# Performance work log

Hardware: AMD Instinct MI355X
Metric: run time of the kernel (lower is better)

The kernel has to match this reference:

```python
import jax, jax.numpy as jnp
import numpy as np
import math

B, L, T, NW, D, DL = 4, 48, 16, 20, 256, 64


def setup_inputs() -> dict:
    key = jax.random.key(0)
    ks = jax.random.split(key, 16)
    n = lambda k, s, sc=1.0: jax.random.normal(k, s, dtype=jnp.float32) * sc
    z = lambda s: jnp.zeros(s, dtype=jnp.float32)
    return {
        'f_c': n(ks[0], (B, L, L, T, D), 0.5),
        'f_m': n(ks[1], (B, L, L, D), 0.5),
        'f_b': n(ks[2], (B, L, D), 0.5),
        'f_w': n(ks[3], (B, NW, D), 0.5),
        'f_s': n(ks[4], (B, D), 0.5),
        'bWq': n(ks[5], (D, D), 0.02), 'bbq': z((D,)),
        'bWk': n(ks[6], (D, D), 0.02), 'bbk': z((D,)),
        'cWq': n(ks[7], (DL, DL), 0.05), 'cbq': z((DL,)),
        'cWk': n(ks[8], (DL, DL), 0.05), 'cbk': z((DL,)),
        'dcc_w': n(ks[9], (DL, D), 0.05), 'dcc_b': z((DL,)),
        'dcw_w': n(ks[10], (DL, D), 0.05), 'dcw_b': z((DL,)),
        'dcs_w': n(ks[11], (DL, D), 0.05), 'dcs_b': z((DL,)),
        'ucc_w': n(ks[12], (D, DL), 0.05), 'ucc_b': z((D,)),
        'mfb_w': n(ks[13], (L, L), 0.05), 'mfb_b': z((L,)),
        'mfc_w': n(ks[14], (L, L), 0.05), 'mfc_b': z((L,)),
    }


def _smi_forward(f_c, f_m, f_b, f_w, f_s, bWq, bbq, bWk, bbk, cWq, cbq, cWk, cbk,
                 dcc_w, dcc_b, dcw_w, dcw_b, dcs_w, dcs_b, ucc_w, ucc_b,
                 mfb_w, mfb_b, mfc_w, mfc_b):
    lin = lambda x, W, b: x @ W.T + b  # torch Linear / 1x1 conv over channel-last

    def boundary_unit(fb, fm):
        # cross attention over words
        q = lin(fb, bWq, bbq)                                   # (B,L,D)
        k = lin(f_w, bWk, bbk)                                  # (B,Nw,D)
        aw = jax.nn.softmax(jnp.einsum('bld,bnd->bln', q, k) / math.sqrt(D), axis=-1)
        f_baq = jnp.einsum('bln,bnd->bld', aw, f_w)
        f_bq = fb * (f_baq + f_s[:, None, :])
        A_b = jax.nn.softmax(jnp.einsum('bld,bmd->blm', f_bq, f_bq) / math.sqrt(D), axis=-1)
        f_bb = jnp.einsum('blm,bmd->bld', A_b, fb)
        g_m = jax.nn.sigmoid(fm * f_s[:, None, None, :])        # (B,L,L,D)
        f_bm = jnp.einsum('blm,blmd->bld', A_b, g_m * fm)
        return f_bb + fb + f_bm

    def content_unit(fc, fm):
        f_c_hat = lin(fc, dcc_w, dcc_b)                         # (B,L,L,T,dl)
        f_w_hat = lin(f_w, dcw_w, dcw_b)                        # (B,Nw,dl)
        f_s_hat = lin(f_s, dcs_w, dcs_b)                        # (B,dl)
        q = lin(f_c_hat, cWq, cbq)
        k = lin(f_w_hat, cWk, cbk)
        aw = jax.nn.softmax(jnp.einsum('blmtd,bnd->blmtn', q, k) / math.sqrt(DL), axis=-1)
        f_caq = jnp.einsum('blmtn,bnd->blmtd', aw, f_w_hat)
        f_cq = f_c_hat * (f_caq + f_s_hat[:, None, None, None, :])
        A_c = jax.nn.softmax(jnp.einsum('blmtd,blmsd->blmts', f_cq, f_cq) / math.sqrt(DL), axis=-1)
        f_cc_hat = jnp.einsum('blmts,blmsd->blmtd', A_c, f_c_hat)
        f_cc = lin(f_cc_hat, ucc_w, ucc_b)                      # (B,L,L,T,D)
        g_m = jax.nn.sigmoid(fm * f_s[:, None, None, :])
        return f_cc + fc + (g_m * fm)[:, :, :, None, :]

    def moment_unit(fc, fm, fb):
        prod = fb[:, :, None, :] * fb[:, None, :, :]            # (B,L,L,D)
        conv_fb = jnp.einsum('oi,bimd->bomd', mfb_w, prod) + mfb_b[None, :, None, None]
        fc_mean = jnp.mean(fc, axis=3)                          # (B,L,L,D)
        conv_fc = jnp.einsum('oi,bimd->bomd', mfc_w, fc_mean) + mfc_b[None, :, None, None]
        return conv_fb + conv_fc + fm

    cu, bu, mu = f_c, f_b, f_m
    for _ in range(3):
        cu_n = content_unit(cu, mu)
        bu_n = boundary_unit(bu, mu)
        mu = moment_unit(cu_n, mu, bu_n)
        cu, bu = cu_n, bu_n
    return (mu, bu)


def reference(f_c, f_m, f_b, f_w, f_s, bWq, bbq, bWk, bbk, cWq, cbq, cWk, cbk,
              dcc_w, dcc_b, dcw_w, dcw_b, dcs_w, dcs_b, ucc_w, ucc_b,
              mfb_w, mfb_b, mfc_w, mfc_b):
    return _smi_forward(f_c, f_m, f_b, f_w, f_s, bWq, bbq, bWk, bbk, cWq, cbq, cWk, cbk,
                        dcc_w, dcc_b, dcw_w, dcw_b, dcs_w, dcs_b, ucc_w, ucc_b,
                        mfb_w, mfb_b, mfc_w, mfc_b)
```

## Files before the change

### kernel.cpp

```cpp
#include <hip/hip_runtime.h>

#define BB 4
#define LL 48
#define TT 16
#define NWW 20
#define DD 256
#define DLL 64

typedef __attribute__((ext_vector_type(8))) short s8v;
typedef __attribute__((ext_vector_type(4))) float f4v;
typedef unsigned short ushort_t;

#define FENCE() asm volatile("" ::: "memory")

#define OFF_CU     0ull
#define OFF_CM     75497472ull
#define OFF_BU0    84934656ull
#define OFF_BU1    85131264ull
#define OFF_FBQ    85327872ull
#define OFF_FWH    85524480ull
#define OFF_FSH    85544960ull
#define OFF_KB     85545984ull
#define OFF_BWQT   85627904ull
#define OFF_WBT    85890048ull
#define OFF_WCT    85899264ull
#define OFF_DCCF   85908480ull
#define OFF_CWQF   85941248ull
#define OFF_UCCF   85949440ull
#define OFF_KCF    85982208ull
#define OFF_FWHTF  85998592ull

static __device__ __forceinline__ ushort_t f2bf(float f){
  unsigned u = __float_as_uint(f);
  return (ushort_t)((u + 0x7FFFu + ((u>>16)&1u)) >> 16);
}
static __device__ __forceinline__ float bf2f(ushort_t h){
  return __uint_as_float(((unsigned)h)<<16);
}
static __device__ __forceinline__ void st64(void* p, float a, float b, float c, float d){
  uint2 v; v.x = (unsigned)f2bf(a) | ((unsigned)f2bf(b)<<16);
  v.y = (unsigned)f2bf(c) | ((unsigned)f2bf(d)<<16);
  *(uint2*)p = v;
}

#define ADR64(row, cb) (((row)<<7) + ((cb) ^ (((row)&7)<<4)))
#define ADR32(row, cb) (((row)<<6) + ((cb) ^ (((row)&3)<<4)))

#define MFMA(a,b,c) __builtin_amdgcn_mfma_f32_16x16x32_bf16((a),(b),(c),0,0,0)

template<int FIRST>
__global__ __launch_bounds__(256)
void content_kernel(const void* cusrc_, ushort_t* cudst, float* __restrict__ cm,
                    const float* __restrict__ fm_src, const float* __restrict__ fsg,
                    const float* __restrict__ fsh, const float* __restrict__ dccb,
                    const float* __restrict__ cbq, const float* __restrict__ uccb,
                    const ushort_t* __restrict__ dccf, const ushort_t* __restrict__ cwqf,
                    const ushort_t* __restrict__ uccf, const ushort_t* __restrict__ kcf,
                    const ushort_t* __restrict__ fwhtf)
{
  __shared__ __align__(16) char sm_all[4][8192];
  const int wid = threadIdx.x >> 6;
  const int lane = threadIdx.x & 63;
  char* sm = sm_all[wid];
  const int t = lane & 15, g = lane >> 4;
  const int tile = blockIdx.x*4 + wid;
  const int b = tile / (LL*LL);

  {
    f4v z = {0.f,0.f,0.f,0.f};
    *(f4v*)(sm + 4096 + ADR32(lane, 32)) = z;
    *(f4v*)(sm + 4096 + ADR32(lane, 48)) = z;
  }

  s8v xb[8];
  if (FIRST){
    const float* xp = (const float*)cusrc_ + (size_t)tile*4096 + t*DD + g*8;
    #pragma unroll
    for (int kk=0;kk<8;kk++){
      f4v lo = *(const f4v*)(xp + kk*32);
      f4v hi = *(const f4v*)(xp + kk*32 + 4);
      s8v v;
      v[0]=(short)f2bf(lo[0]); v[1]=(short)f2bf(lo[1]);
      v[2]=(short)f2bf(lo[2]); v[3]=(short)f2bf(lo[3]);
      v[4]=(short)f2bf(hi[0]); v[5]=(short)f2bf(hi[1]);
      v[6]=(short)f2bf(hi[2]); v[7]=(short)f2bf(hi[3]);
      xb[kk]=v;
    }
  } else {
    const ushort_t* xp = (const ushort_t*)cusrc_ + (size_t)tile*4096 + lane*8;
    #pragma unroll
    for (int kk=0;kk<8;kk++) xb[kk] = *(const s8v*)(xp + kk*512);
  }

  f4v accH[4];
  {
    f4v z = {0.f,0.f,0.f,0.f};
    accH[0]=z; accH[1]=z; accH[2]=z; accH[3]=z;
  }
  #pragma unroll
  for (int kk=0;kk<8;kk++){
    #pragma unroll
    for (int m0=0;m0<4;m0++){
      s8v a = *(const s8v*)(dccf + (((m0<<3)+kk)<<9) + (lane<<3));
      accH[m0] = MFMA(a, xb[kk], accH[m0]);
    }
  }
  s8v cwa[8];
  #pragma unroll
  for (int i=0;i<8;i++) cwa[i] = *(const s8v*)(cwqf + (i<<9) + (lane<<3));
  #pragma unroll
  for (int m0=0;m0<4;m0++){
    f4v acc = accH[m0];
    f4v bi = *(const f4v*)(dccb + m0*16 + g*4);
    acc[0]+=bi[0]; acc[1]+=bi[1]; acc[2]+=bi[2]; acc[3]+=bi[3];
    accH[m0]=acc;
    st64(sm + ADR64(t, m0*32 + g*8), acc[0],acc[1],acc[2],acc[3]);
    #pragma unroll
    for (int r=0;r<4;r++)
      *(ushort_t*)(sm + 4096 + ADR32(m0*16 + g*4 + r, t*2)) = f2bf(acc[r]);
  }
  FENCE();

  s8v hb0 = *(const s8v*)(sm + ADR64(t, g*16));
  s8v hb1 = *(const s8v*)(sm + ADR64(t, 64 + g*16));
  #pragma unroll
  for (int m0=0;m0<4;m0++){
    f4v acc = {0.f,0.f,0.f,0.f};
    acc = MFMA(cwa[m0*2  ], hb0, acc);
    acc = MFMA(cwa[m0*2+1], hb1, acc);
    f4v bi = *(const f4v*)(cbq + m0*16 + g*4);
    st64(sm + 2048 + ADR64(t, m0*32 + g*8),
         acc[0]+bi[0], acc[1]+bi[1], acc[2]+bi[2], acc[3]+bi[3]);
  }
  s8v kca[4];
  #pragma unroll
  for (int i=0;i<4;i++) kca[i] = *(const s8v*)(kcf + (b<<11) + (i<<9) + (lane<<3));
  FENCE();

  s8v qb0 = *(const s8v*)(sm + 2048 + ADR64(t, g*16));
  s8v qb1 = *(const s8v*)(sm + 2048 + ADR64(t, 64 + g*16));
  f4v sA[2];
  #pragma unroll
  for (int m0=0;m0<2;m0++){
    f4v acc = {0.f,0.f,0.f,0.f};
    acc = MFMA(kca[m0*2  ], qb0, acc);
    acc = MFMA(kca[m0*2+1], qb1, acc);
    sA[m0]=acc;
  }
  float mx = -3.0e38f;
  #pragma unroll
  for (int m0=0;m0<2;m0++){
    #pragma unroll
    for (int r=0;r<4;r++){
      int n = m0*16 + g*4 + r;
      if (n < NWW) mx = fmaxf(mx, sA[m0][r]);
    }
  }
  mx = fmaxf(mx, __shfl_xor(mx, 16));
  mx = fmaxf(mx, __shfl_xor(mx, 32));
  float ex[8]; float sum = 0.f;
  #pragma unroll
  for (int m0=0;m0<2;m0++){
    #pragma unroll
    for (int r=0;r<4;r++){
      int n = m0*16 + g*4 + r;
      float e = (n < NWW) ? __expf(sA[m0][r]-mx) : 0.f;
      ex[m0*4+r]=e; sum+=e;
    }
  }
  sum += __shfl_xor(sum,16);
  sum += __shfl_xor(sum,32);
  float inv = 1.f/sum;
  #pragma unroll
  for (int m0=0;m0<2;m0++)
    st64(sm + ADR32(t, m0*32 + g*8),
         ex[m0*4]*inv, ex[m0*4+1]*inv, ex[m0*4+2]*inv, ex[m0*4+3]*inv);
  s8v fwa[4];
  #pragma unroll
  for (int i=0;i<4;i++) fwa[i] = *(const s8v*)(fwhtf + (b<<11) + (i<<9) + (lane<<3));
  FENCE();

  s8v awb = *(const s8v*)(sm + ADR32(t, g*16));
  FENCE();
  #pragma unroll
  for (int m0=0;m0<4;m0++){
    f4v z = {0.f,0.f,0.f,0.f};
    f4v acc = MFMA(fwa[m0], awb, z);
    f4v fv = *(const f4v*)(fsh + b*DLL + m0*16 + g*4);
    float cq0 = accH[m0][0]*(acc[0]+fv[0])*0.35355339059f;
    float cq1 = accH[m0][1]*(acc[1]+fv[1])*0.35355339059f;
    float cq2 = accH[m0][2]*(acc[2]+fv[2])*0.35355339059f;
    float cq3 = accH[m0][3]*(acc[3]+fv[3])*0.35355339059f;
    ushort_t h0=f2bf(cq0),h1=f2bf(cq1),h2=f2bf(cq2),h3=f2bf(cq3);
    uint2 hv; hv.x=(unsigned)h0|((unsigned)h1<<16); hv.y=(unsigned)h2|((unsigned)h3<<16);
    *(uint2*)(sm + 2048 + ADR64(t, m0*32+g*8)) = hv;
    uint2 lv;
    lv.x = (unsigned)f2bf(cq0-bf2f(h0)) | ((unsigned)f2bf(cq1-bf2f(h1))<<16);
    lv.y = (unsigned)f2bf(cq2-bf2f(h2)) | ((unsigned)f2bf(cq3-bf2f(h3))<<16);
    *(uint2*)(sm + ADR64(t, m0*32+g*8)) = lv;
  }
  FENCE();

  s8v ch0 = *(const s8v*)(sm + 2048 + ADR64(t, g*16));
  s8v ch1 = *(const s8v*)(sm + 2048 + ADR64(t, 64+g*16));
  s8v cl0 = *(const s8v*)(sm + ADR64(t, g*16));
  s8v cl1 = *(const s8v*)(sm + ADR64(t, 64+g*16));
  f4v s2 = {0.f,0.f,0.f,0.f};
  s2 = MFMA(ch0, ch0, s2); s2 = MFMA(ch1, ch1, s2);
  s2 = MFMA(ch0, cl0, s2); s2 = MFMA(ch1, cl1, s2);
  s2 = MFMA(cl0, ch0, s2); s2 = MFMA(cl1, ch1, s2);
  float mx2 = fmaxf(fmaxf(s2[0],s2[1]), fmaxf(s2[2],s2[3]));
  mx2 = fmaxf(mx2, __shfl_xor(mx2,16));
  mx2 = fmaxf(mx2, __shfl_xor(mx2,32));
  float e0=__expf(s2[0]-mx2), e1=__expf(s2[1]-mx2), e2=__expf(s2[2]-mx2), e3=__expf(s2[3]-mx2);
  float su = e0+e1+e2+e3;
  su += __shfl_xor(su,16);
  su += __shfl_xor(su,32);
  float inv2 = 1.f/su;
  FENCE();
  st64(sm + ADR32(t, g*8), e0*inv2, e1*inv2, e2*inv2, e3*inv2);
  { uint2 zz; zz.x=0u; zz.y=0u; *(uint2*)(sm + ADR32(t, 32+g*8)) = zz; }
  FENCE();

  s8v acb = *(const s8v*)(sm + ADR32(t, g*16));
  #pragma unroll
  for (int m0=0;m0<4;m0++){
    s8v a = *(const s8v*)(sm + 4096 + ADR32(m0*16 + t, g*16));
    f4v z = {0.f,0.f,0.f,0.f};
    f4v acc = MFMA(a, acb, z);
    st64(sm + 2048 + ADR64(t, m0*32+g*8), acc[0],acc[1],acc[2],acc[3]);
  }
  FENCE();

  s8v cc0 = *(const s8v*)(sm + 2048 + ADR64(t, g*16));
  s8v cc1 = *(const s8v*)(sm + 2048 + ADR64(t, 64+g*16));
  FENCE();
  const float* fmp = fm_src + (size_t)tile*DD;
  const float* fsp = fsg + b*DD;
  const int frofs = t*8 + (g>>1)*128 + (g&1)*4;
  const ushort_t* xfr = (const ushort_t*)cusrc_ + (size_t)tile*4096 + frofs;
  ushort_t* ofr = cudst + (size_t)tile*4096 + frofs;
  const float* xf = (const float*)cusrc_ + (size_t)tile*4096 + t*DD;
  #pragma unroll
  for (int m0=0;m0<16;m0++){
    f4v acc = {0.f,0.f,0.f,0.f};
    s8v a0 = *(const s8v*)(uccf + (((m0<<1)  )<<9) + (lane<<3));
    s8v a1 = *(const s8v*)(uccf + (((m0<<1)+1)<<9) + (lane<<3));
    acc = MFMA(a0, cc0, acc);
    acc = MFMA(a1, cc1, acc);
    const int dq = m0*16 + g*4;
    const int fi = (m0>>1)*512 + (m0&1)*256;
    f4v ub  = *(const f4v*)(uccb + dq);
    f4v fmv = *(const f4v*)(fmp + dq);
    f4v fvv = *(const f4v*)(fsp + dq);
    float xr0,xr1,xr2,xr3;
    if (FIRST){
      f4v xv = *(const f4v*)(xf + dq);
      xr0=xv[0]; xr1=xv[1]; xr2=xv[2]; xr3=xv[3];
    } else {
      uint2 xv = *(const uint2*)(xfr + fi);
      xr0=bf2f((ushort_t)(xv.x&0xffffu)); xr1=bf2f((ushort_t)(xv.x>>16));
      xr2=bf2f((ushort_t)(xv.y&0xffffu)); xr3=bf2f((ushort_t)(xv.y>>16));
    }
    float o0 = acc[0]+ub[0]+xr0 + fmv[0]*__builtin_amdgcn_rcpf(1.f+__expf(-fmv[0]*fvv[0]));
    float o1 = acc[1]+ub[1]+xr1 + fmv[1]*__builtin_amdgcn_rcpf(1.f+__expf(-fmv[1]*fvv[1]));
    float o2 = acc[2]+ub[2]+xr2 + fmv[2]*__builtin_amdgcn_rcpf(1.f+__expf(-fmv[2]*fvv[2]));
    float o3 = acc[3]+ub[3]+xr3 + fmv[3]*__builtin_amdgcn_rcpf(1.f+__expf(-fmv[3]*fvv[3]));
    uint2 ov; ov.x=(unsigned)f2bf(o0)|((unsigned)f2bf(o1)<<16);
    ov.y=(unsigned)f2bf(o2)|((unsigned)f2bf(o3)<<16);
    *(uint2*)(ofr + fi) = ov;
    *(uint2*)(sm + (t<<9) + ((dq*2) ^ ((t&15)<<3))) = ov;
  }
  FENCE();

  {
    const int d0 = lane*4;
    float s0=0.f,s1=0.f,s2=0.f,s3=0.f;
    #pragma unroll
    for (int tt=0;tt<TT;tt++){
      uint2 v = *(const uint2*)(sm + (tt<<9) + ((d0*2) ^ ((tt&15)<<3)));
      s0 += bf2f((ushort_t)(v.x&0xffffu)); s1 += bf2f((ushort_t)(v.x>>16));
      s2 += bf2f((ushort_t)(v.y&0xffffu)); s3 += bf2f((ushort_t)(v.y>>16));
    }
    f4v o = {s0*0.0625f, s1*0.0625f, s2*0.0625f, s3*0.0625f};
    *(f4v*)(cm + (size_t)tile*DD + d0) = o;
  }
}

__global__ __launch_bounds__(256)
void bnd1_kernel(const float* __restrict__ fb, const float* __restrict__ f_w,
                 const float* __restrict__ f_s, const float* __restrict__ kb,
                 const float* __restrict__ bWqT, const float* __restrict__ bbq,
                 float* __restrict__ fbq)
{
  int blk = blockIdx.x; int b = blk / LL, l = blk % LL;
  int d = threadIdx.x;
  __shared__ float fbrow[DD];
  __shared__ float qrow[DD];
  __shared__ float smx[32];
  fbrow[d] = fb[(size_t)(b*LL+l)*DD + d];
  __syncthreads();
  float q = bbq[d];
  for (int e=0;e<DD;e++) q += fbrow[e]*bWqT[(size_t)e*DD+d];
  qrow[d]=q;
  __syncthreads();
  if (d < NWW){
    float s=0.f; const float* kr = kb + (size_t)(b*NWW+d)*DD;
    for (int e=0;e<DD;e++) s += qrow[e]*kr[e];
    smx[d] = s*(1.0f/16.0f);
  }
  __syncthreads();
  if (d==0){
    float m2=-3.0e38f;
    for(int n=0;n<NWW;n++) m2=fmaxf(m2,smx[n]);
    float su=0.f;
    for(int n=0;n<NWW;n++){ float e=__expf(smx[n]-m2); smx[n]=e; su+=e; }
    float iv=1.f/su;
    for(int n=0;n<NWW;n++) smx[n]*=iv;
  }
  __syncthreads();
  float acc=0.f;
  for (int n=0;n<NWW;n++) acc += smx[n]*f_w[(size_t)(b*NWW+n)*DD+d];
  fbq[(size_t)(b*LL+l)*DD+d] = fbrow[d]*(acc + f_s[b*DD+d]);
}

__global__ __launch_bounds__(256)
void bnd2_kernel(const float* __restrict__ fbq, const float* __restrict__ fb,
                 const float* __restrict__ fm, const float* __restrict__ f_s,
                 float* __restrict__ bu_out)
{
  int blk = blockIdx.x; int b = blk/LL, l = blk%LL;
  int d = threadIdx.x;
  __shared__ float Sl[DD];
  __shared__ float aw[LL];
  Sl[d] = fbq[(size_t)(b*LL+l)*DD + d];
  __syncthreads();
  if (d < LL){
    float s=0.f; const float* fr = fbq + (size_t)(b*LL+d)*DD;
    const f4v* s4 = (const f4v*)Sl; const f4v* f4p = (const f4v*)fr;
    for (int e=0;e<DD/4;e++){
      f4v a=s4[e], c=f4p[e];
      s += a[0]*c[0]+a[1]*c[1]+a[2]*c[2]+a[3]*c[3];
    }
    aw[d] = s*(1.0f/16.0f);
  }
  __syncthreads();
  if (d==0){
    float m2=-3.0e38f;
    for(int n=0;n<LL;n++) m2=fmaxf(m2,aw[n]);
    float su=0.f;
    for(int n=0;n<LL;n++){ float e=__expf(aw[n]-m2); aw[n]=e; su+=e; }
    float iv=1.f/su;
    for(int n=0;n<LL;n++) aw[n]*=iv;
  }
  __syncthreads();
  float fsd = f_s[b*DD+d];
  const float* fmrow = fm + ((size_t)(b*LL+l)*LL)*DD + d;
  float acc=0.f;
  for (int m=0;m<LL;m++){
    float a  = aw[m];
    float fbv= fb[(size_t)(b*LL+m)*DD+d];
    float fmv= fmrow[(size_t)m*DD];
    float gm = 1.f/(1.f+__expf(-fmv*fsd));
    acc += a*(fbv + gm*fmv);
  }
  bu_out[(size_t)(b*LL+l)*DD+d] = acc + fb[(size_t)(b*LL+l)*DD+d];
}

__global__ __launch_bounds__(256)
void moment_kernel(const float* __restrict__ cm, const float* __restrict__ bu,
                   const float* __restrict__ mu_in, float* __restrict__ mu_out,
                   const float* __restrict__ wbT, const float* __restrict__ wcT,
                   const float* __restrict__ mfbb, const float* __restrict__ mfcb)
{
  int blk = blockIdx.x;
  int oh = blk & 1; int bm = blk>>1; int b = bm/LL, m = bm%LL;
  int d = threadIdx.x;
  const int ob = oh*24;
  float accB[24], accC[24];
  #pragma unroll
  for (int o=0;o<24;o++){accB[o]=0.f;accC[o]=0.f;}
  for (int i=0;i<LL;i++){
    float bv = bu[(size_t)(b*LL+i)*DD+d];
    float cv = cm[((size_t)(b*LL+i)*LL+m)*DD+d];
    const float* wb = wbT + i*LL + ob;
    const float* wc = wcT + i*LL + ob;
    #pragma unroll
    for (int o=0;o<24;o+=4){
      f4v w1 = *(const f4v*)(wb+o);
      f4v w2 = *(const f4v*)(wc+o);
      accB[o  ]+=w1[0]*bv; accB[o+1]+=w1[1]*bv; accB[o+2]+=w1[2]*bv; accB[o+3]+=w1[3]*bv;
      accC[o  ]+=w2[0]*cv; accC[o+1]+=w2[1]*cv; accC[o+2]+=w2[2]*cv; accC[o+3]+=w2[3]*cv;
    }
  }
  float bum = bu[(size_t)(b*LL+m)*DD+d];
  #pragma unroll
  for (int o=0;o<24;o++){
    int oo = ob+o;
    size_t oi = ((size_t)(b*LL+oo)*LL+m)*DD + d;
    mu_out[oi] = accB[o]*bum + mfbb[oo] + accC[o] + mfcb[oo] + mu_in[oi];
  }
}

__global__ __launch_bounds__(256)
void prep1_kernel(const float* __restrict__ f_w, const float* __restrict__ f_s,
                  const float* __restrict__ bWq, const float* __restrict__ bWk,
                  const float* __restrict__ bbk,
                  const float* __restrict__ dcw_w, const float* __restrict__ dcw_b,
                  const float* __restrict__ dcs_w, const float* __restrict__ dcs_b,
                  const float* __restrict__ dcc_w, const float* __restrict__ cWq,
                  const float* __restrict__ ucc_w,
                  const float* __restrict__ mfb_w, const float* __restrict__ mfc_w,
                  float* __restrict__ kb, float* __restrict__ fwh,
                  float* __restrict__ fsh, float* __restrict__ bWqT,
                  ushort_t* __restrict__ dccf, ushort_t* __restrict__ cwqf,
                  ushort_t* __restrict__ uccf,
                  float* __restrict__ wbT, float* __restrict__ wcT)
{
  const int S0=20480, S1=5120, S2=256, S3=65536, S4=16384, S5=4096, S6=16384, S7=2304;
  const int TOT = S0+S1+S2+S3+S4+S5+S6+S7;
  int id = blockIdx.x*256 + threadIdx.x;
  int nth = gridDim.x*256;
  for (int x=id; x<TOT; x+=nth){
    int y=x;
    if (y < S0){
      int b=y/(NWW*DD); int r=y%(NWW*DD); int n=r/DD, dd2=r%DD;
      float s=bbk[dd2];
      const float* fr=f_w+(size_t)(b*NWW+n)*DD; const float* wr=bWk+(size_t)dd2*DD;
      for(int e=0;e<DD;e++) s+=fr[e]*wr[e];
      kb[y]=s; continue; }
    y-=S0;
    if (y < S1){
      int b=y/(NWW*DLL); int r=y%(NWW*DLL); int n=r/DLL, dl=r%DLL;
      float s=dcw_b[dl];
      const float* fr=f_w+(size_t)(b*NWW+n)*DD; const float* wr=dcw_w+(size_t)dl*DD;
      for(int e=0;e<DD;e++) s+=fr[e]*wr[e];
      fwh[y]=s; continue; }
    y-=S1;
    if (y < S2){
      int b=y/DLL, dl=y%DLL;
      float s=dcs_b[dl];
      const float* fr=f_s+(size_t)b*DD; const float* wr=dcs_w+(size_t)dl*DD;
      for(int e=0;e<DD;e++) s+=fr[e]*wr[e];
      fsh[y]=s; continue; }
    y-=S2;
    if (y < S3){ int e=y/DD, dd2=y%DD; bWqT[y] = bWq[(size_t)dd2*DD+e]; continue; }
    y-=S3;
    if (y < S4){
      int j=y&7, ln=(y>>3)&63, kk=(y>>9)&7, m0=y>>12;
      int mm=m0*16+(ln&15), k=kk*32+((ln>>4)<<3)+j;
      dccf[y]=f2bf(dcc_w[(size_t)mm*DD+k]); continue; }
    y-=S4;
    if (y < S5){
      int j=y&7, ln=(y>>3)&63, kk=(y>>9)&1, m0=y>>10;
      int mm=m0*16+(ln&15), k=kk*32+((ln>>4)<<3)+j;
      cwqf[y]=f2bf(cWq[(size_t)mm*DLL+k]); continue; }
    y-=S5;
    if (y < S6){
      int j=y&7, ln=(y>>3)&63, kk=(y>>9)&1, m0=y>>10;
      int mm=m0*16+(ln&15), k=kk*32+((ln>>4)<<3)+j;
      uccf[y]=f2bf(ucc_w[(size_t)mm*DLL+k]); continue; }
    y-=S6;
    { int i=y/LL, o=y%LL; wbT[y]=mfb_w[(size_t)o*LL+i]; wcT[y]=mfc_w[(size_t)o*LL+i]; }
  }
}

__global__ __launch_bounds__(256)
void prep2_kernel(const float* __restrict__ fwh, const float* __restrict__ cWk,
                  const float* __restrict__ cbk,
                  ushort_t* __restrict__ kcf, ushort_t* __restrict__ fwhtf)
{
  const int S0 = BB*2048, S1 = BB*2048;
  int id = blockIdx.x*256+threadIdx.x; int nth=gridDim.x*256;
  for (int x=id; x<S0+S1; x+=nth){
    int y=x;
    if (y < S0){
      int b=y>>11; int z=y&2047;
      int j=z&7, ln=(z>>3)&63, kk=(z>>9)&1, m0=z>>10;
      int n=m0*16+(ln&15), k=kk*32+((ln>>4)<<3)+j;
      float v=0.f;
      if (n<NWW){
        float s=cbk[k];
        const float* fr=fwh+(size_t)(b*NWW+n)*DLL; const float* wr=cWk+(size_t)k*DLL;
        for(int e=0;e<DLL;e++) s+=fr[e]*wr[e];
        v=s*0.125f;
      }
      kcf[y]=f2bf(v); continue; }
    y-=S0;
    {
      int b=y>>11; int z=y&2047;
      int j=z&7, ln=(z>>3)&63, m0=z>>9;
      int dl=m0*16+(ln&15), n=((ln>>4)<<3)+j;
      float v = (n<NWW)? fwh[(size_t)(b*NWW+n)*DLL+dl] : 0.f;
      fwhtf[y]=f2bf(v);
    }
  }
}

extern "C" void kernel_launch(void* const* d_in, const int* in_sizes, int n_in,
                              void* d_out, int out_size, void* d_ws, size_t ws_size,
                              hipStream_t stream)
{
  (void)in_sizes; (void)n_in; (void)out_size; (void)ws_size;
  const float* f_c  = (const float*)d_in[0];
  const float* f_m  = (const float*)d_in[1];
  const float* f_b  = (const float*)d_in[2];
  const float* f_w  = (const float*)d_in[3];
  const float* f_s  = (const float*)d_in[4];
  const float* bWq  = (const float*)d_in[5];
  const float* bbq  = (const float*)d_in[6];
  const float* bWk  = (const float*)d_in[7];
  const float* bbk  = (const float*)d_in[8];
  const float* cWq  = (const float*)d_in[9];
  const float* cbq  = (const float*)d_in[10];
  const float* cWk  = (const float*)d_in[11];
  const float* cbk  = (const float*)d_in[12];
  const float* dcc_w= (const float*)d_in[13];
  const float* dcc_b= (const float*)d_in[14];
  const float* dcw_w= (const float*)d_in[15];
  const float* dcw_b= (const float*)d_in[16];
  const float* dcs_w= (const float*)d_in[17];
  const float* dcs_b= (const float*)d_in[18];
  const float* ucc_w= (const float*)d_in[19];
  const float* ucc_b= (const float*)d_in[20];
  const float* mfb_w= (const float*)d_in[21];
  const float* mfb_b= (const float*)d_in[22];
  const float* mfc_w= (const float*)d_in[23];
  const float* mfc_b= (const float*)d_in[24];

  char* ws = (char*)d_ws;
  ushort_t* cu = (ushort_t*)(ws+OFF_CU);
  float* cmr  = (float*)(ws+OFF_CM);
  float* bu0  = (float*)(ws+OFF_BU0);
  float* bu1  = (float*)(ws+OFF_BU1);
  float* fbq  = (float*)(ws+OFF_FBQ);
  float* fwh  = (float*)(ws+OFF_FWH);
  float* fsh  = (float*)(ws+OFF_FSH);
  float* kb   = (float*)(ws+OFF_KB);
  float* bWqT = (float*)(ws+OFF_BWQT);
  float* wbT  = (float*)(ws+OFF_WBT);
  float* wcT  = (float*)(ws+OFF_WCT);
  ushort_t* dccf = (ushort_t*)(ws+OFF_DCCF);
  ushort_t* cwqf = (ushort_t*)(ws+OFF_CWQF);
  ushort_t* uccf = (ushort_t*)(ws+OFF_UCCF);
  ushort_t* kcf  = (ushort_t*)(ws+OFF_KCF);
  ushort_t* fwhtf= (ushort_t*)(ws+OFF_FWHTF);

  float* mu = (float*)d_out;
  float* out_bu = (float*)d_out + 2359296;

  prep1_kernel<<<128,256,0,stream>>>(f_w,f_s,bWq,bWk,bbk,dcw_w,dcw_b,dcs_w,dcs_b,
                                     dcc_w,cWq,ucc_w,mfb_w,mfc_w,
                                     kb,fwh,fsh,bWqT,dccf,cwqf,uccf,wbT,wcT);
  prep2_kernel<<<32,256,0,stream>>>(fwh,cWk,cbk,kcf,fwhtf);

  float* bu_cur = nullptr;
  for (int it=0; it<3; ++it){
    const float* fmsrc = (it==0)? f_m : mu;
    if (it==0)
      content_kernel<1><<<2304,256,0,stream>>>(f_c, cu, cmr, fmsrc, f_s, fsh, dcc_b, cbq, ucc_b,
                                               dccf,cwqf,uccf,kcf,fwhtf);
    else
      content_kernel<0><<<2304,256,0,stream>>>(cu, cu, cmr, fmsrc, f_s, fsh, dcc_b, cbq, ucc_b,
                                               dccf,cwqf,uccf,kcf,fwhtf);
    const float* fbsrc = (it==0)? f_b : bu_cur;
    float* bunew = (it==2)? out_bu : ((it==0)? bu0 : ((bu_cur==bu0)? bu1 : bu0));
    bnd1_kernel<<<192,256,0,stream>>>(fbsrc, f_w, f_s, kb, bWqT, bbq, fbq);
    bnd2_kernel<<<192,256,0,stream>>>(fbq, fbsrc, fmsrc, f_s, bunew);
    moment_kernel<<<384,256,0,stream>>>(cmr, bunew, fmsrc, mu, wbT, wcT, mfb_b, mfc_b);
    bu_cur = bunew;
  }
}
```

Measured before the change: 388.0 us.

## Process two tiles per wavefront in content kernel to reuse weight fragments

Each wavefront in the content kernel now handles two (b,l,m) tiles instead of one, and blocks shrink from 256 to 128 threads while the grid size stays the same. Weight fragments such as dccf, cwqf, uccf, kcf and fwhtf are loaded once and fed to MFMAs for both tiles. This halves global and L2 weight traffic per tile and gives each wave two independent MFMA chains to interleave. The cost is roughly double the register pressure, which may lower occupancy, and fewer waves per block.

```diff
diff --git a/kernel.cpp b/kernel.cpp
--- a/kernel.cpp
+++ b/kernel.cpp
@@ -49,7 +49,7 @@
 #define MFMA(a,b,c) __builtin_amdgcn_mfma_f32_16x16x32_bf16((a),(b),(c),0,0,0)
 
 template<int FIRST>
-__global__ __launch_bounds__(256)
+__global__ __launch_bounds__(128)
 void content_kernel(const void* cusrc_, ushort_t* cudst, float* __restrict__ cm,
                     const float* __restrict__ fm_src, const float* __restrict__ fsg,
                     const float* __restrict__ fsh, const float* __restrict__ dccb,
@@ -61,48 +61,62 @@
   __shared__ __align__(16) char sm_all[4][8192];
   const int wid = threadIdx.x >> 6;
   const int lane = threadIdx.x & 63;
-  char* sm = sm_all[wid];
+  char* smA = sm_all[wid*2];
+  char* smB = sm_all[wid*2+1];
   const int t = lane & 15, g = lane >> 4;
-  const int tile = blockIdx.x*4 + wid;
-  const int b = tile / (LL*LL);
-
-  {
-    f4v z = {0.f,0.f,0.f,0.f};
-    *(f4v*)(sm + 4096 + ADR32(lane, 32)) = z;
-    *(f4v*)(sm + 4096 + ADR32(lane, 48)) = z;
-  }
-
-  s8v xb[8];
+  const int tileA = blockIdx.x*4 + wid*2;
+  const int tileB = tileA + 1;
+  const int b = tileA / (LL*LL);
+
+  { f4v z = {0.f,0.f,0.f,0.f};
+    *(f4v*)(smA + 4096 + ADR32(lane, 32)) = z;
+    *(f4v*)(smA + 4096 + ADR32(lane, 48)) = z;
+    *(f4v*)(smB + 4096 + ADR32(lane, 32)) = z;
+    *(f4v*)(smB + 4096 + ADR32(lane, 48)) = z; }
+
+  s8v xbA[8], xbB[8];
   if (FIRST){
-    const float* xp = (const float*)cusrc_ + (size_t)tile*4096 + t*DD + g*8;
+    const float* xpA = (const float*)cusrc_ + (size_t)tileA*4096 + t*DD + g*8;
+    const float* xpB = (const float*)cusrc_ + (size_t)tileB*4096 + t*DD + g*8;
     #pragma unroll
     for (int kk=0;kk<8;kk++){
-      f4v lo = *(const f4v*)(xp + kk*32);
-      f4v hi = *(const f4v*)(xp + kk*32 + 4);
+      f4v lo = *(const f4v*)(xpA + kk*32);
+      f4v hi = *(const f4v*)(xpA + kk*32 + 4);
       s8v v;
       v[0]=(short)f2bf(lo[0]); v[1]=(short)f2bf(lo[1]);
       v[2]=(short)f2bf(lo[2]); v[3]=(short)f2bf(lo[3]);
       v[4]=(short)f2bf(hi[0]); v[5]=(short)f2bf(hi[1]);
       v[6]=(short)f2bf(hi[2]); v[7]=(short)f2bf(hi[3]);
-      xb[kk]=v;
+      xbA[kk]=v;
+      lo = *(const f4v*)(xpB + kk*32);
+      hi = *(const f4v*)(xpB + kk*32 + 4);
+      v[0]=(short)f2bf(lo[0]); v[1]=(short)f2bf(lo[1]);
+      v[2]=(short)f2bf(lo[2]); v[3]=(short)f2bf(lo[3]);
+      v[4]=(short)f2bf(hi[0]); v[5]=(short)f2bf(hi[1]);
+      v[6]=(short)f2bf(hi[2]); v[7]=(short)f2bf(hi[3]);
+      xbB[kk]=v;
     }
   } else {
-    const ushort_t* xp = (const ushort_t*)cusrc_ + (size_t)tile*4096 + lane*8;
-    #pragma unroll
-    for (int kk=0;kk<8;kk++) xb[kk] = *(const s8v*)(xp + kk*512);
-  }
-
-  f4v accH[4];
-  {
-    f4v z = {0.f,0.f,0.f,0.f};
-    accH[0]=z; accH[1]=z; accH[2]=z; accH[3]=z;
-  }
+    const ushort_t* xpA = (const ushort_t*)cusrc_ + (size_t)tileA*4096 + lane*8;
+    const ushort_t* xpB = (const ushort_t*)cusrc_ + (size_t)tileB*4096 + lane*8;
+    #pragma unroll
+    for (int kk=0;kk<8;kk++){
+      xbA[kk] = *(const s8v*)(xpA + kk*512);
+      xbB[kk] = *(const s8v*)(xpB + kk*512);
+    }
+  }
+
+  f4v accHA[4], accHB[4];
+  { f4v z = {0.f,0.f,0.f,0.f};
+    accHA[0]=z;accHA[1]=z;accHA[2]=z;accHA[3]=z;
+    accHB[0]=z;accHB[1]=z;accHB[2]=z;accHB[3]=z; }
   #pragma unroll
   for (int kk=0;kk<8;kk++){
     #pragma unroll
     for (int m0=0;m0<4;m0++){
       s8v a = *(const s8v*)(dccf + (((m0<<3)+kk)<<9) + (lane<<3));
-      accH[m0] = MFMA(a, xb[kk], accH[m0]);
+      accHA[m0] = MFMA(a, xbA[kk], accHA[m0]);
+      accHB[m0] = MFMA(a, xbB[kk], accHB[m0]);
     }
   }
   s8v cwa[8];
@@ -110,180 +124,278 @@
   for (int i=0;i<8;i++) cwa[i] = *(const s8v*)(cwqf + (i<<9) + (lane<<3));
   #pragma unroll
   for (int m0=0;m0<4;m0++){
-    f4v acc = accH[m0];
     f4v bi = *(const f4v*)(dccb + m0*16 + g*4);
-    acc[0]+=bi[0]; acc[1]+=bi[1]; acc[2]+=bi[2]; acc[3]+=bi[3];
-    accH[m0]=acc;
-    st64(sm + ADR64(t, m0*32 + g*8), acc[0],acc[1],acc[2],acc[3]);
-    #pragma unroll
-    for (int r=0;r<4;r++)
-      *(ushort_t*)(sm + 4096 + ADR32(m0*16 + g*4 + r, t*2)) = f2bf(acc[r]);
-  }
-  FENCE();
-
-  s8v hb0 = *(const s8v*)(sm + ADR64(t, g*16));
-  s8v hb1 = *(const s8v*)(sm + ADR64(t, 64 + g*16));
+    f4v a1 = accHA[m0];
+    a1[0]+=bi[0]; a1[1]+=bi[1]; a1[2]+=bi[2]; a1[3]+=bi[3];
+    accHA[m0]=a1;
+    st64(smA + ADR64(t, m0*32 + g*8), a1[0],a1[1],a1[2],a1[3]);
+    f4v a2 = accHB[m0];
+    a2[0]+=bi[0]; a2[1]+=bi[1]; a2[2]+=bi[2]; a2[3]+=bi[3];
+    accHB[m0]=a2;
+    st64(smB + ADR64(t, m0*32 + g*8), a2[0],a2[1],a2[2],a2[3]);
+    #pragma unroll
+    for (int r=0;r<4;r++){
+      *(ushort_t*)(smA + 4096 + ADR32(m0*16 + g*4 + r, t*2)) = f2bf(a1[r]);
+      *(ushort_t*)(smB + 4096 + ADR32(m0*16 + g*4 + r, t*2)) = f2bf(a2[r]);
+    }
+  }
+  FENCE();
+
+  s8v hbA0 = *(const s8v*)(smA + ADR64(t, g*16));
+  s8v hbA1 = *(const s8v*)(smA + ADR64(t, 64 + g*16));
+  s8v hbB0 = *(const s8v*)(smB + ADR64(t, g*16));
+  s8v hbB1 = *(const s8v*)(smB + ADR64(t, 64 + g*16));
   #pragma unroll
   for (int m0=0;m0<4;m0++){
-    f4v acc = {0.f,0.f,0.f,0.f};
-    acc = MFMA(cwa[m0*2  ], hb0, acc);
-    acc = MFMA(cwa[m0*2+1], hb1, acc);
     f4v bi = *(const f4v*)(cbq + m0*16 + g*4);
-    st64(sm + 2048 + ADR64(t, m0*32 + g*8),
-         acc[0]+bi[0], acc[1]+bi[1], acc[2]+bi[2], acc[3]+bi[3]);
+    f4v aa = {0.f,0.f,0.f,0.f};
+    aa = MFMA(cwa[m0*2  ], hbA0, aa);
+    aa = MFMA(cwa[m0*2+1], hbA1, aa);
+    st64(smA + 2048 + ADR64(t, m0*32 + g*8),
+         aa[0]+bi[0], aa[1]+bi[1], aa[2]+bi[2], aa[3]+bi[3]);
+    f4v ab = {0.f,0.f,0.f,0.f};
+    ab = MFMA(cwa[m0*2  ], hbB0, ab);
+    ab = MFMA(cwa[m0*2+1], hbB1, ab);
+    st64(smB + 2048 + ADR64(t, m0*32 + g*8),
+         ab[0]+bi[0], ab[1]+bi[1], ab[2]+bi[2], ab[3]+bi[3]);
   }
   s8v kca[4];
   #pragma unroll
   for (int i=0;i<4;i++) kca[i] = *(const s8v*)(kcf + (b<<11) + (i<<9) + (lane<<3));
   FENCE();
 
-  s8v qb0 = *(const s8v*)(sm + 2048 + ADR64(t, g*16));
-  s8v qb1 = *(const s8v*)(sm + 2048 + ADR64(t, 64 + g*16));
-  f4v sA[2];
+  s8v qbA0 = *(const s8v*)(smA + 2048 + ADR64(t, g*16));
+  s8v qbA1 = *(const s8v*)(smA + 2048 + ADR64(t, 64 + g*16));
+  s8v qbB0 = *(const s8v*)(smB + 2048 + ADR64(t, g*16));
+  s8v qbB1 = *(const s8v*)(smB + 2048 + ADR64(t, 64 + g*16));
+  f4v sAA[2], sAB[2];
   #pragma unroll
   for (int m0=0;m0<2;m0++){
-    f4v acc = {0.f,0.f,0.f,0.f};
-    acc = MFMA(kca[m0*2  ], qb0, acc);
-    acc = MFMA(kca[m0*2+1], qb1, acc);
-    sA[m0]=acc;
-  }
-  float mx = -3.0e38f;
-  #pragma unroll
-  for (int m0=0;m0<2;m0++){
-    #pragma unroll
-    for (int r=0;r<4;r++){
-      int n = m0*16 + g*4 + r;
-      if (n < NWW) mx = fmaxf(mx, sA[m0][r]);
-    }
-  }
-  mx = fmaxf(mx, __shfl_xor(mx, 16));
-  mx = fmaxf(mx, __shfl_xor(mx, 32));
-  float ex[8]; float sum = 0.f;
-  #pragma unroll
-  for (int m0=0;m0<2;m0++){
-    #pragma unroll
-    for (int r=0;r<4;r++){
-      int n = m0*16 + g*4 + r;
-      float e = (n < NWW) ? __expf(sA[m0][r]-mx) : 0.f;
-      ex[m0*4+r]=e; sum+=e;
-    }
-  }
-  sum += __shfl_xor(sum,16);
-  sum += __shfl_xor(sum,32);
-  float inv = 1.f/sum;
-  #pragma unroll
-  for (int m0=0;m0<2;m0++)
-    st64(sm + ADR32(t, m0*32 + g*8),
-         ex[m0*4]*inv, ex[m0*4+1]*inv, ex[m0*4+2]*inv, ex[m0*4+3]*inv);
+    f4v aa = {0.f,0.f,0.f,0.f};
+    aa = MFMA(kca[m0*2  ], qbA0, aa);
+    aa = MFMA(kca[m0*2+1], qbA1, aa);
+    sAA[m0]=aa;
+    f4v ab = {0.f,0.f,0.f,0.f};
+    ab = MFMA(kca[m0*2  ], qbB0, ab);
+    ab = MFMA(kca[m0*2+1], qbB1, ab);
+    sAB[m0]=ab;
+  }
+  {
+    float mxA = -3.0e38f, mxB = -3.0e38f;
+    #pragma unroll
+    for (int m0=0;m0<2;m0++){
+      #pragma unroll
+      for (int r=0;r<4;r++){
+        int n = m0*16 + g*4 + r;
+        if (n < NWW){ mxA = fmaxf(mxA, sAA[m0][r]); mxB = fmaxf(mxB, sAB[m0][r]); }
+      }
+    }
+    mxA = fmaxf(mxA, __shfl_xor(mxA, 16)); mxA = fmaxf(mxA, __shfl_xor(mxA, 32));
+    mxB = fmaxf(mxB, __shfl_xor(mxB, 16)); mxB = fmaxf(mxB, __shfl_xor(mxB, 32));
+    float exA[8], exB[8]; float suA = 0.f, suB = 0.f;
+    #pragma unroll
+    for (int m0=0;m0<2;m0++){
+      #pragma unroll
+      for (int r=0;r<4;r++){
+        int n = m0*16 + g*4 + r;
+        float eA = (n < NWW) ? __expf(sAA[m0][r]-mxA) : 0.f;
+        float eB = (n < NWW) ? __expf(sAB[m0][r]-mxB) : 0.f;
+        exA[m0*4+r]=eA; suA+=eA;
+        exB[m0*4+r]=eB; suB+=eB;
+      }
+    }
+    suA += __shfl_xor(suA,16); suA += __shfl_xor(suA,32);
+    suB += __shfl_xor(suB,16); suB += __shfl_xor(suB,32);
+    float ivA = 1.f/suA, ivB = 1.f/suB;
+    #pragma unroll
+    for (int m0=0;m0<2;m0++){
+      st64(smA + ADR32(t, m0*32 + g*8),
+           exA[m0*4]*ivA, exA[m0*4+1]*ivA, exA[m0*4+2]*ivA, exA[m0*4+3]*ivA);
+      st64(smB + ADR32(t, m0*32 + g*8),
+           exB[m0*4]*ivB, exB[m0*4+1]*ivB, exB[m0*4+2]*ivB, exB[m0*4+3]*ivB);
+    }
+  }
   s8v fwa[4];
   #pragma unroll
   for (int i=0;i<4;i++) fwa[i] = *(const s8v*)(fwhtf + (b<<11) + (i<<9) + (lane<<3));
   FENCE();
 
-  s8v awb = *(const s8v*)(sm + ADR32(t, g*16));
+  s8v awbA = *(const s8v*)(smA + ADR32(t, g*16));
+  s8v awbB = *(const s8v*)(smB + ADR32(t, g*16));
   FENCE();
   #pragma unroll
   for (int m0=0;m0<4;m0++){
     f4v z = {0.f,0.f,0.f,0.f};
-    f4v acc = MFMA(fwa[m0], awb, z);
     f4v fv = *(const f4v*)(fsh + b*DLL + m0*16 + g*4);
-    float cq0 = accH[m0][0]*(acc[0]+fv[0])*0.35355339059f;
-    float cq1 = accH[m0][1]*(acc[1]+fv[1])*0.35355339059f;
-    float cq2 = accH[m0][2]*(acc[2]+fv[2])*0.35355339059f;
-    float cq3 = accH[m0][3]*(acc[3]+fv[3])*0.35355339059f;
-    ushort_t h0=f2bf(cq0),h1=f2bf(cq1),h2=f2bf(cq2),h3=f2bf(cq3);
-    uint2 hv; hv.x=(unsigned)h0|((unsigned)h1<<16); hv.y=(unsigned)h2|((unsigned)h3<<16);
-    *(uint2*)(sm + 2048 + ADR64(t, m0*32+g*8)) = hv;
-    uint2 lv;
-    lv.x = (unsigned)f2bf(cq0-bf2f(h0)) | ((unsigned)f2bf(cq1-bf2f(h1))<<16);
-    lv.y = (unsigned)f2bf(cq2-bf2f(h2)) | ((unsigned)f2bf(cq3-bf2f(h3))<<16);
-    *(uint2*)(sm + ADR64(t, m0*32+g*8)) = lv;
-  }
-  FENCE();
-
-  s8v ch0 = *(const s8v*)(sm + 2048 + ADR64(t, g*16));
-  s8v ch1 = *(const s8v*)(sm + 2048 + ADR64(t, 64+g*16));
-  s8v cl0 = *(const s8v*)(sm + ADR64(t, g*16));
-  s8v cl1 = *(const s8v*)(sm + ADR64(t, 64+g*16));
-  f4v s2 = {0.f,0.f,0.f,0.f};
-  s2 = MFMA(ch0, ch0, s2); s2 = MFMA(ch1, ch1, s2);
-  s2 = MFMA(ch0, cl0, s2); s2 = MFMA(ch1, cl1, s2);
-  s2 = MFMA(cl0, ch0, s2); s2 = MFMA(cl1, ch1, s2);
-  float mx2 = fmaxf(fmaxf(s2[0],s2[1]), fmaxf(s2[2],s2[3]));
-  mx2 = fmaxf(mx2, __shfl_xor(mx2,16));
-  mx2 = fmaxf(mx2, __shfl_xor(mx2,32));
-  float e0=__expf(s2[0]-mx2), e1=__expf(s2[1]-mx2), e2=__expf(s2[2]-mx2), e3=__expf(s2[3]-mx2);
-  float su = e0+e1+e2+e3;
-  su += __shfl_xor(su,16);
-  su += __shfl_xor(su,32);
-  float inv2 = 1.f/su;
-  FENCE();
-  st64(sm + ADR32(t, g*8), e0*inv2, e1*inv2, e2*inv2, e3*inv2);
-  { uint2 zz; zz.x=0u; zz.y=0u; *(uint2*)(sm + ADR32(t, 32+g*8)) = zz; }
-  FENCE();
-
-  s8v acb = *(const s8v*)(sm + ADR32(t, g*16));
-  #pragma unroll
-  for (int m0=0;m0<4;m0++){
-    s8v a = *(const s8v*)(sm + 4096 + ADR32(m0*16 + t, g*16));
-    f4v z = {0.f,0.f,0.f,0.f};
-    f4v acc = MFMA(a, acb, z);
-    st64(sm + 2048 + ADR64(t, m0*32+g*8), acc[0],acc[1],acc[2],acc[3]);
-  }
-  FENCE();
-
-  s8v cc0 = *(const s8v*)(sm + 2048 + ADR64(t, g*16));
-  s8v cc1 = *(const s8v*)(sm + 2048 + ADR64(t, 64+g*16));
-  FENCE();
-  const float* fmp = fm_src + (size_t)tile*DD;
+    f4v aa = MFMA(fwa[m0], awbA, z);
+    f4v ab = MFMA(fwa[m0], awbB, z);
+    {
+      float c0 = accHA[m0][0]*(aa[0]+fv[0])*0.35355339059f;
+      float c1 = accHA[m0][1]*(aa[1]+fv[1])*0.35355339059f;
+      float c2 = accHA[m0][2]*(aa[2]+fv[2])*0.35355339059f;
+      float c3 = accHA[m0][3]*(aa[3]+fv[3])*0.35355339059f;
+      ushort_t h0=f2bf(c0),h1=f2bf(c1),h2=f2bf(c2),h3=f2bf(c3);
+      uint2 hv; hv.x=(unsigned)h0|((unsigned)h1<<16); hv.y=(unsigned)h2|((unsigned)h3<<16);
+      *(uint2*)(smA + 2048 + ADR64(t, m0*32+g*8)) = hv;
+      uint2 lv;
+      lv.x = (unsigned)f2bf(c0-bf2f(h0)) | ((unsigned)f2bf(c1-bf2f(h1))<<16);
+      lv.y = (unsigned)f2bf(c2-bf2f(h2)) | ((unsigned)f2bf(c3-bf2f(h3))<<16);
+      *(uint2*)(smA + ADR64(t, m0*32+g*8)) = lv;
+    }
+    {
+      float c0 = accHB[m0][0]*(ab[0]+fv[0])*0.35355339059f;
+      float c1 = accHB[m0][1]*(ab[1]+fv[1])*0.35355339059f;
+      float c2 = accHB[m0][2]*(ab[2]+fv[2])*0.35355339059f;
+      float c3 = accHB[m0][3]*(ab[3]+fv[3])*0.35355339059f;
+      ushort_t h0=f2bf(c0),h1=f2bf(c1),h2=f2bf(c2),h3=f2bf(c3);
+      uint2 hv; hv.x=(unsigned)h0|((unsigned)h1<<16); hv.y=(unsigned)h2|((unsigned)h3<<16);
+      *(uint2*)(smB + 2048 + ADR64(t, m0*32+g*8)) = hv;
+      uint2 lv;
+      lv.x = (unsigned)f2bf(c0-bf2f(h0)) | ((unsigned)f2bf(c1-bf2f(h1))<<16);
+      lv.y = (unsigned)f2bf(c2-bf2f(h2)) | ((unsigned)f2bf(c3-bf2f(h3))<<16);
+      *(uint2*)(smB + ADR64(t, m0*32+g*8)) = lv;
+    }
+  }
+  FENCE();
+
+  {
+    s8v chA0 = *(const s8v*)(smA + 2048 + ADR64(t, g*16));
+    s8v chA1 = *(const s8v*)(smA + 2048 + ADR64(t, 64+g*16));
+    s8v clA0 = *(const s8v*)(smA + ADR64(t, g*16));
+    s8v clA1 = *(const s8v*)(smA + ADR64(t, 64+g*16));
+    s8v chB0 = *(const s8v*)(smB + 2048 + ADR64(t, g*16));
+    s8v chB1 = *(const s8v*)(smB + 2048 + ADR64(t, 64+g*16));
+    s8v clB0 = *(const s8v*)(smB + ADR64(t, g*16));
+    s8v clB1 = *(const s8v*)(smB + ADR64(t, 64+g*16));
+    f4v s2A = {0.f,0.f,0.f,0.f};
+    s2A = MFMA(chA0, chA0, s2A); s2A = MFMA(chA1, chA1, s2A);
+    s2A = MFMA(chA0, clA0, s2A); s2A = MFMA(chA1, clA1, s2A);
+    s2A = MFMA(clA0, chA0, s2A); s2A = MFMA(clA1, chA1, s2A);
+    f4v s2B = {0.f,0.f,0.f,0.f};
+    s2B = MFMA(chB0, chB0, s2B); s2B = MFMA(chB1, chB1, s2B);
+    s2B = MFMA(chB0, clB0, s2B); s2B = MFMA(chB1, clB1, s2B);
+    s2B = MFMA(clB0, chB0, s2B); s2B = MFMA(clB1, chB1, s2B);
+    float mA = fmaxf(fmaxf(s2A[0],s2A[1]), fmaxf(s2A[2],s2A[3]));
+    mA = fmaxf(mA, __shfl_xor(mA,16)); mA = fmaxf(mA, __shfl_xor(mA,32));
+    float mB = fmaxf(fmaxf(s2B[0],s2B[1]), fmaxf(s2B[2],s2B[3]));
+    mB = fmaxf(mB, __shfl_xor(mB,16)); mB = fmaxf(mB, __shfl_xor(mB,32));
+    float eA0=__expf(s2A[0]-mA), eA1=__expf(s2A[1]-mA), eA2=__expf(s2A[2]-mA), eA3=__expf(s2A[3]-mA);
+    float eB0=__expf(s2B[0]-mB), eB1=__expf(s2B[1]-mB), eB2=__expf(s2B[2]-mB), eB3=__expf(s2B[3]-mB);
+    float sA_ = eA0+eA1+eA2+eA3; sA_ += __shfl_xor(sA_,16); sA_ += __shfl_xor(sA_,32);
+    float sB_ = eB0+eB1+eB2+eB3; sB_ += __shfl_xor(sB_,16); sB_ += __shfl_xor(sB_,32);
+    float iA = 1.f/sA_, iB = 1.f/sB_;
+    FENCE();
+    st64(smA + ADR32(t, g*8), eA0*iA, eA1*iA, eA2*iA, eA3*iA);
+    st64(smB + ADR32(t, g*8), eB0*iB, eB1*iB, eB2*iB, eB3*iB);
+    uint2 zz; zz.x=0u; zz.y=0u;
+    *(uint2*)(smA + ADR32(t, 32+g*8)) = zz;
+    *(uint2*)(smB + ADR32(t, 32+g*8)) = zz;
+  }
+  FENCE();
+
+  {
+    s8v acbA = *(const s8v*)(smA + ADR32(t, g*16));
+    s8v acbB = *(const s8v*)(smB + ADR32(t, g*16));
+    #pragma unroll
+    for (int m0=0;m0<4;m0++){
+      f4v z = {0.f,0.f,0.f,0.f};
+      s8v aA = *(const s8v*)(smA + 4096 + ADR32(m0*16 + t, g*16));
+      f4v ra = MFMA(aA, acbA, z);
+      st64(smA + 2048 + ADR64(t, m0*32+g*8), ra[0],ra[1],ra[2],ra[3]);
+      s8v aB = *(const s8v*)(smB + 4096 + ADR32(m0*16 + t, g*16));
+      f4v rb = MFMA(aB, acbB, z);
+      st64(smB + 2048 + ADR64(t, m0*32+g*8), rb[0],rb[1],rb[2],rb[3]);
+    }
+  }
+  FENCE();
+
+  s8v ccA0 = *(const s8v*)(smA + 2048 + ADR64(t, g*16));
+  s8v ccA1 = *(const s8v*)(smA + 2048 + ADR64(t, 64+g*16));
+  s8v ccB0 = *(const s8v*)(smB + 2048 + ADR64(t, g*16));
+  s8v ccB1 = *(const s8v*)(smB + 2048 + ADR64(t, 64+g*16));
+  FENCE();
+  const float* fmpA = fm_src + (size_t)tileA*DD;
+  const float* fmpB = fm_src + (size_t)tileB*DD;
   const float* fsp = fsg + b*DD;
   const int frofs = t*8 + (g>>1)*128 + (g&1)*4;
-  const ushort_t* xfr = (const ushort_t*)cusrc_ + (size_t)tile*4096 + frofs;
-  ushort_t* ofr = cudst + (size_t)tile*4096 + frofs;
-  const float* xf = (const float*)cusrc_ + (size_t)tile*4096 + t*DD;
+  const ushort_t* xfrA = (const ushort_t*)cusrc_ + (size_t)tileA*4096 + frofs;
+  const ushort_t* xfrB = (const ushort_t*)cusrc_ + (size_t)tileB*4096 + frofs;
+  ushort_t* ofrA = cudst + (size_t)tileA*4096 + frofs;
+  ushort_t* ofrB = cudst + (size_t)tileB*4096 + frofs;
+  const float* xfA = (const float*)cusrc_ + (size_t)tileA*4096 + t*DD;
+  const float* xfB = (const float*)cusrc_ + (size_t)tileB*4096 + t*DD;
   #pragma unroll
   for (int m0=0;m0<16;m0++){
-    f4v acc = {0.f,0.f,0.f,0.f};
     s8v a0 = *(const s8v*)(uccf + (((m0<<1)  )<<9) + (lane<<3));
     s8v a1 = *(const s8v*)(uccf + (((m0<<1)+1)<<9) + (lane<<3));
-    acc = MFMA(a0, cc0, acc);
-    acc = MFMA(a1, cc1, acc);
+    f4v accA = {0.f,0.f,0.f,0.f};
+    accA = MFMA(a0, ccA0, accA); accA = MFMA(a1, ccA1, accA);
+    f4v accB = {0.f,0.f,0.f,0.f};
+    accB = MFMA(a0, ccB0, accB); accB = MFMA(a1, ccB1, accB);
     const int dq = m0*16 + g*4;
     const int fi = (m0>>1)*512 + (m0&1)*256;
     f4v ub  = *(const f4v*)(uccb + dq);
-    f4v fmv = *(const f4v*)(fmp + dq);
     f4v fvv = *(const f4v*)(fsp + dq);
-    float xr0,xr1,xr2,xr3;
-    if (FIRST){
-      f4v xv = *(const f4v*)(xf + dq);
-      xr0=xv[0]; xr1=xv[1]; xr2=xv[2]; xr3=xv[3];
-    } else {
-      uint2 xv = *(const uint2*)(xfr + fi);
-      xr0=bf2f((ushort_t)(xv.x&0xffffu)); xr1=bf2f((ushort_t)(xv.x>>16));
-      xr2=bf2f((ushort_t)(xv.y&0xffffu)); xr3=bf2f((ushort_t)(xv.y>>16));
-    }
-    float o0 = acc[0]+ub[0]+xr0 + fmv[0]*__builtin_amdgcn_rcpf(1.f+__expf(-fmv[0]*fvv[0]));
-    float o1 = acc[1]+ub[1]+xr1 + fmv[1]*__builtin_amdgcn_rcpf(1.f+__expf(-fmv[1]*fvv[1]));
-    float o2 = acc[2]+ub[2]+xr2 + fmv[2]*__builtin_amdgcn_rcpf(1.f+__expf(-fmv[2]*fvv[2]));
-    float o3 = acc[3]+ub[3]+xr3 + fmv[3]*__builtin_amdgcn_rcpf(1.f+__expf(-fmv[3]*fvv[3]));
-    uint2 ov; ov.x=(unsigned)f2bf(o0)|((unsigned)f2bf(o1)<<16);
-    ov.y=(unsigned)f2bf(o2)|((unsigned)f2bf(o3)<<16);
-    *(uint2*)(ofr + fi) = ov;
-    *(uint2*)(sm + (t<<9) + ((dq*2) ^ ((t&15)<<3))) = ov;
+    {
+      f4v fmv = *(const f4v*)(fmpA + dq);
+      float xr0,xr1,xr2,xr3;
+      if (FIRST){
+        f4v xv = *(const f4v*)(xfA + dq);
+        xr0=xv[0]; xr1=xv[1]; xr2=xv[2]; xr3=xv[3];
+      } else {
+        uint2 xv = *(const uint2*)(xfrA + fi);
+        xr0=bf2f((ushort_t)(xv.x&0xffffu)); xr1=bf2f((ushort_t)(xv.x>>16));
+        xr2=bf2f((ushort_t)(xv.y&0xffffu)); xr3=bf2f((ushort_t)(xv.y>>16));
+      }
+      float o0 = accA[0]+ub[0]+xr0 + fmv[0]*__builtin_amdgcn_rcpf(1.f+__expf(-fmv[0]*fvv[0]));
+      float o1 = accA[1]+ub[1]+xr1 + fmv[1]*__builtin_amdgcn_rcpf(1.f+__expf(-fmv[1]*fvv[1]));
+      float o2 = accA[2]+ub[2]+xr2 + fmv[2]*__builtin_amdgcn_rcpf(1.f+__expf(-fmv[2]*fvv[2]));
+      float o3 = accA[3]+ub[3]+xr3 + fmv[3]*__builtin_amdgcn_rcpf(1.f+__expf(-fmv[3]*fvv[3]));
+      uint2 ov; ov.x=(unsigned)f2bf(o0)|((unsigned)f2bf(o1)<<16);
+      ov.y=(unsigned)f2bf(o2)|((unsigned)f2bf(o3)<<16);
+      *(uint2*)(ofrA + fi) = ov;
+      *(uint2*)(smA + (t<<9) + ((dq*2) ^ ((t&15)<<3))) = ov;
+    }
+    {
+      f4v fmv = *(const f4v*)(fmpB + dq);
+      float xr0,xr1,xr2,xr3;
+      if (FIRST){
+        f4v xv = *(const f4v*)(xfB + dq);
+        xr0=xv[0]; xr1=xv[1]; xr2=xv[2]; xr3=xv[3];
+      } else {
+        uint2 xv = *(const uint2*)(xfrB + fi);
+        xr0=bf2f((ushort_t)(xv.x&0xffffu)); xr1=bf2f((ushort_t)(xv.x>>16));
+        xr2=bf2f((ushort_t)(xv.y&0xffffu)); xr3=bf2f((ushort_t)(xv.y>>16));
+      }
+      float o0 = accB[0]+ub[0]+xr0 + fmv[0]*__builtin_amdgcn_rcpf(1.f+__expf(-fmv[0]*fvv[0]));
+      float o1 = accB[1]+ub[1]+xr1 + fmv[1]*__builtin_amdgcn_rcpf(1.f+__expf(-fmv[1]*fvv[1]));
+      float o2 = accB[2]+ub[2]+xr2 + fmv[2]*__builtin_amdgcn_rcpf(1.f+__expf(-fmv[2]*fvv[2]));
+      float o3 = accB[3]+ub[3]+xr3 + fmv[3]*__builtin_amdgcn_rcpf(1.f+__expf(-fmv[3]*fvv[3]));
+      uint2 ov; ov.x=(unsigned)f2bf(o0)|((unsigned)f2bf(o1)<<16);
+      ov.y=(unsigned)f2bf(o2)|((unsigned)f2bf(o3)<<16);
+      *(uint2*)(ofrB + fi) = ov;
+      *(uint2*)(smB + (t<<9) + ((dq*2) ^ ((t&15)<<3))) = ov;
+    }
   }
   FENCE();
 
   {
     const int d0 = lane*4;
-    float s0=0.f,s1=0.f,s2=0.f,s3=0.f;
+    float a0=0.f,a1=0.f,a2=0.f,a3=0.f;
+    float b0=0.f,b1=0.f,b2=0.f,b3=0.f;
     #pragma unroll
     for (int tt=0;tt<TT;tt++){
-      uint2 v = *(const uint2*)(sm + (tt<<9) + ((d0*2) ^ ((tt&15)<<3)));
-      s0 += bf2f((ushort_t)(v.x&0xffffu)); s1 += bf2f((ushort_t)(v.x>>16));
-      s2 += bf2f((ushort_t)(v.y&0xffffu)); s3 += bf2f((ushort_t)(v.y>>16));
-    }
-    f4v o = {s0*0.0625f, s1*0.0625f, s2*0.0625f, s3*0.0625f};
-    *(f4v*)(cm + (size_t)tile*DD + d0) = o;
+      uint2 v = *(const uint2*)(smA + (tt<<9) + ((d0*2) ^ ((tt&15)<<3)));
+      a0 += bf2f((ushort_t)(v.x&0xffffu)); a1 += bf2f((ushort_t)(v.x>>16));
+      a2 += bf2f((ushort_t)(v.y&0xffffu)); a3 += bf2f((ushort_t)(v.y>>16));
+      uint2 w = *(const uint2*)(smB + (tt<<9) + ((d0*2) ^ ((tt&15)<<3)));
+      b0 += bf2f((ushort_t)(w.x&0xffffu)); b1 += bf2f((ushort_t)(w.x>>16));
+      b2 += bf2f((ushort_t)(w.y&0xffffu)); b3 += bf2f((ushort_t)(w.y>>16));
+    }
+    f4v oa = {a0*0.0625f, a1*0.0625f, a2*0.0625f, a3*0.0625f};
+    *(f4v*)(cm + (size_t)tileA*DD + d0) = oa;
+    f4v ob = {b0*0.0625f, b1*0.0625f, b2*0.0625f, b3*0.0625f};
+    *(f4v*)(cm + (size_t)tileB*DD + d0) = ob;
   }
 }
 
@@ -558,10 +670,10 @@
   for (int it=0; it<3; ++it){
     const float* fmsrc = (it==0)? f_m : mu;
     if (it==0)
-      content_kernel<1><<<2304,256,0,stream>>>(f_c, cu, cmr, fmsrc, f_s, fsh, dcc_b, cbq, ucc_b,
+      content_kernel<1><<<2304,128,0,stream>>>(f_c, cu, cmr, fmsrc, f_s, fsh, dcc_b, cbq, ucc_b,
                                                dccf,cwqf,uccf,kcf,fwhtf);
     else
-      content_kernel<0><<<2304,256,0,stream>>>(cu, cu, cmr, fmsrc, f_s, fsh, dcc_b, cbq, ucc_b,
+      content_kernel<0><<<2304,128,0,stream>>>(cu, cu, cmr, fmsrc, f_s, fsh, dcc_b, cbq, ucc_b,
                                                dccf,cwqf,uccf,kcf,fwhtf);
     const float* fbsrc = (it==0)? f_b : bu_cur;
     float* bunew = (it==2)? out_bu : ((it==0)? bu0 : ((bu_cur==bu0)? bu1 : bu0));
```

Result: slower. 477.2 us (+23.0%).
